# Optimization experiments

Hardware: AMD Instinct MI355X
Metric: run time of the kernel (lower is better)

## Reference

```python
import jax, jax.numpy as jnp
import numpy as np

B, T, S = 4, 1024, 1024
E, H, D, M = 768, 12, 64, 3072
SCALE = 1.0 / (D ** 0.5)
EPS = 1e-5


def setup_inputs() -> dict:
    key = jax.random.key(0)
    ks = jax.random.split(key, 20)
    s = 0.02

    def n(k, shp):
        return jax.random.normal(k, shp, jnp.float32) * s

    return {
        "target": jax.random.normal(ks[0], (B, T, E), jnp.float32),
        "memory": jax.random.normal(ks[1], (B, S, E), jnp.float32),
        # self-attention: per-head Q/K/V projections stacked over heads [H,E,D]
        "sa_wq": n(ks[2], (H, E, D)), "sa_bq": jnp.zeros((H, D), jnp.float32),
        "sa_wk": n(ks[3], (H, E, D)), "sa_bk": jnp.zeros((H, D), jnp.float32),
        "sa_wv": n(ks[4], (H, E, D)), "sa_bv": jnp.zeros((H, D), jnp.float32),
        "sa_wo": n(ks[5], (H * D, E)), "sa_bo": jnp.zeros((E,), jnp.float32),
        # cross-attention
        "ca_wq": n(ks[6], (H, E, D)), "ca_bq": jnp.zeros((H, D), jnp.float32),
        "ca_wk": n(ks[7], (H, E, D)), "ca_bk": jnp.zeros((H, D), jnp.float32),
        "ca_wv": n(ks[8], (H, E, D)), "ca_bv": jnp.zeros((H, D), jnp.float32),
        "ca_wo": n(ks[9], (H * D, E)), "ca_bo": jnp.zeros((E,), jnp.float32),
        # layernorms
        "ln1_g": jnp.ones((E,), jnp.float32), "ln1_b": jnp.zeros((E,), jnp.float32),
        "ln2_g": jnp.ones((E,), jnp.float32), "ln2_b": jnp.zeros((E,), jnp.float32),
        "ln3_g": jnp.ones((E,), jnp.float32), "ln3_b": jnp.zeros((E,), jnp.float32),
        # FFN
        "ffn_w1": n(ks[10], (E, M)), "ffn_b1": jnp.zeros((M,), jnp.float32),
        "ffn_w2": n(ks[11], (M, E)), "ffn_b2": jnp.zeros((E,), jnp.float32),
    }


def layernorm(x, g, b):
    mu = jnp.mean(x, axis=-1, keepdims=True)
    var = jnp.mean(jnp.square(x - mu), axis=-1, keepdims=True)
    return (x - mu) * jax.lax.rsqrt(var + EPS) * g + b


def mha(q_in, k_in, v_in, wq, bq, wk, bk, wv, bv, wo, bo, mask=None):
    # batched equivalent of the per-head looped projections
    Q = jnp.einsum('bse,hed->bhsd', q_in, wq) + bq[None, :, None, :]
    K = jnp.einsum('bte,hed->bhtd', k_in, wk) + bk[None, :, None, :]
    V = jnp.einsum('bte,hed->bhtd', v_in, wv) + bv[None, :, None, :]
    scores = jnp.einsum('bhsd,bhtd->bhst', Q, K) * SCALE
    if mask is not None:
        scores = jnp.where(mask, scores, -jnp.inf)
    w = jax.nn.softmax(scores, axis=-1)
    o = jnp.einsum('bhst,bhtd->bhsd', w, V)  # [B,H,Sq,D]
    o = o.transpose(0, 2, 1, 3).reshape(q_in.shape[0], q_in.shape[1], H * D)
    return o @ wo + bo


def reference(target, memory,
              sa_wq, sa_bq, sa_wk, sa_bk, sa_wv, sa_bv, sa_wo, sa_bo,
              ca_wq, ca_bq, ca_wk, ca_bk, ca_wv, ca_bv, ca_wo, ca_bo,
              ln1_g, ln1_b, ln2_g, ln2_b, ln3_g, ln3_b,
              ffn_w1, ffn_b1, ffn_w2, ffn_b2):
    Tq = target.shape[1]
    causal = jnp.tril(jnp.ones((Tq, Tq), bool))  # [T,T], broadcasts over B,H
    # pre-norm self-attention + residual
    x = layernorm(target, ln1_g, ln1_b)
    x = mha(x, x, x, sa_wq, sa_bq, sa_wk, sa_bk, sa_wv, sa_bv, sa_wo, sa_bo, causal) + target
    # pre-norm cross-attention + residual
    res = x
    y = layernorm(x, ln2_g, ln2_b)
    x = mha(y, memory, memory, ca_wq, ca_bq, ca_wk, ca_bk, ca_wv, ca_bv, ca_wo, ca_bo) + res
    # pre-norm FFN (Linear -> GELU -> Linear) + residual
    res = x
    y = layernorm(x, ln3_g, ln3_b)
    x = jax.nn.gelu(y @ ffn_w1 + ffn_b1) @ ffn_w2 + ffn_b2 + res
    return x
```

## Files before the change

kernel.cpp:

```cpp
#include <hip/hip_runtime.h>
#include <hip/hip_bf16.h>
#include <stdint.h>

#define BB 4
#define TT 1024
#define SS 1024
#define EE 768
#define HH 12
#define DDIM 64
#define MM 3072
#define NROWS 4096
#define ATT_SCALE 0.125f

typedef unsigned short u16;
using short8 = __attribute__((ext_vector_type(8))) short;
using f32x4  = __attribute__((ext_vector_type(4))) float;

__device__ inline f32x4 mfma16(short8 a, short8 b, f32x4 c) {
  return __builtin_amdgcn_mfma_f32_16x16x32_bf16(a, b, c, 0, 0, 0);
}

__device__ inline float b2f(u16 u) {
  union { uint32_t i; float f; } z; z.i = ((uint32_t)u) << 16; return z.f;
}
__device__ inline u16 f2b(float f) {
  __hip_bfloat16 h = __float2bfloat16(f);
  return *reinterpret_cast<u16*>(&h);
}
__device__ inline float loadf(const float* p) { return *p; }
__device__ inline float loadf(const u16* p) { return b2f(*p); }

__device__ inline float gelu_f(float x) {
  const float k0 = 0.7978845608028654f;
  const float k1 = 0.044715f;
  float t = tanhf(k0 * (x + k1 * x * x * x));
  return 0.5f * x * (1.0f + t);
}

__device__ inline void gload16(const u16* g, u16* l) {
  __builtin_amdgcn_global_load_lds(
      (const __attribute__((address_space(1))) unsigned int*)g,
      (__attribute__((address_space(3))) unsigned int*)l, 16, 0, 0);
}

__global__ __launch_bounds__(256) void prep_k(
    const float* __restrict__ target, const float* __restrict__ ln1_g,
    const float* __restrict__ ln1_b, u16* __restrict__ lnb,
    const float* __restrict__ mem, u16* __restrict__ memB,
    const float* __restrict__ bq3, const float* __restrict__ bk3,
    const float* __restrict__ bv3, float* __restrict__ d3,
    const float* __restrict__ bk2, const float* __restrict__ bv2,
    float* __restrict__ d2,
    const float* __restrict__ sa_wq, const float* __restrict__ sa_wk,
    const float* __restrict__ sa_wv, u16* __restrict__ wqkvT_sa,
    const float* __restrict__ ca_wq, const float* __restrict__ ca_wk,
    const float* __restrict__ ca_wv, u16* __restrict__ wqkvT_ca,
    const float* __restrict__ sa_wo, const float* __restrict__ ca_wo,
    u16* __restrict__ woT,
    const float* __restrict__ ffn_w1, u16* __restrict__ w1T,
    const float* __restrict__ ffn_w2, u16* __restrict__ w2T) {
  __shared__ u16 tile[32][34];
  __shared__ float red[8];
  const int blk = blockIdx.x, t = threadIdx.x;
  if (blk < 4096) {
    const float* xr = target + (size_t)blk * EE;
    float v0 = xr[t], v1 = xr[t + 256], v2 = xr[t + 512];
    float s = v0 + v1 + v2;
#pragma unroll
    for (int m = 32; m >= 1; m >>= 1) s += __shfl_xor(s, m);
    int wv = t >> 6, ln = t & 63;
    if (ln == 0) red[wv] = s;
    __syncthreads();
    float mean = (red[0] + red[1] + red[2] + red[3]) * (1.0f / EE);
    float e0 = v0 - mean, e1 = v1 - mean, e2 = v2 - mean;
    float s2 = e0 * e0 + e1 * e1 + e2 * e2;
#pragma unroll
    for (int m = 32; m >= 1; m >>= 1) s2 += __shfl_xor(s2, m);
    if (ln == 0) red[4 + wv] = s2;
    __syncthreads();
    float var = (red[4] + red[5] + red[6] + red[7]) * (1.0f / EE);
    float rstd = rsqrtf(var + 1e-5f);
    u16* yr = lnb + (size_t)blk * EE;
    yr[t]       = f2b(e0 * rstd * ln1_g[t]       + ln1_b[t]);
    yr[t + 256] = f2b(e1 * rstd * ln1_g[t + 256] + ln1_b[t + 256]);
    yr[t + 512] = f2b(e2 * rstd * ln1_g[t + 512] + ln1_b[t + 512]);
  } else if (blk < 7168) {
    int i = ((blk - 4096) * 256 + t) * 4;
    float4 f = *(const float4*)(mem + i);
    u16 o[4] = {f2b(f.x), f2b(f.y), f2b(f.z), f2b(f.w)};
    *(uint64_t*)(memB + i) = *(const uint64_t*)o;
  } else if (blk < 7177) {
    int i = (blk - 7168) * 256 + t;
    if (i < 768) d3[i] = bq3[i];
    else if (i < 1536) d3[i] = bk3[i - 768];
    else d3[i] = bv3[i - 1536];
  } else if (blk < 7183) {
    int i = (blk - 7177) * 256 + t;
    if (i < 768) d2[i] = bk2[i];
    else d2[i] = bv2[i - 768];
  } else {
    const float* ip; u16* op; int R, C, bx, by;
    int r = blk - 7183;
    if (r < 1728) {
      int u = r / 48, rr = r % 48; bx = rr & 1; by = rr >> 1;
      const float* s = (u < 12) ? sa_wq : (u < 24) ? sa_wk : sa_wv;
      ip = s + (size_t)(u % 12) * EE * DDIM;
      op = wqkvT_sa + (size_t)u * EE * DDIM;
      R = EE; C = DDIM;
    } else if (r < 3456) {
      r -= 1728;
      int u = r / 48, rr = r % 48; bx = rr & 1; by = rr >> 1;
      const float* s = (u < 12) ? ca_wq : (u < 24) ? ca_wk : ca_wv;
      ip = s + (size_t)(u % 12) * EE * DDIM;
      op = wqkvT_ca + (size_t)u * EE * DDIM;
      R = EE; C = DDIM;
    } else if (r < 4608) {
      r -= 3456;
      int u = r / 576, rr = r % 576; bx = rr % 24; by = rr / 24;
      ip = (u == 0) ? sa_wo : ca_wo;
      op = woT + (size_t)u * EE * EE;
      R = EE; C = EE;
    } else if (r < 6912) {
      r -= 4608; bx = r % 96; by = r / 96;
      ip = ffn_w1; op = w1T; R = EE; C = MM;
    } else {
      r -= 6912; bx = r % 24; by = r / 24;
      ip = ffn_w2; op = w2T; R = MM; C = EE;
    }
    int r0 = by * 32, c0 = bx * 32;
    int tx = t & 31, ty = t >> 5;
#pragma unroll
    for (int j = 0; j < 32; j += 8)
      tile[ty + j][tx] = f2b(ip[(size_t)(r0 + ty + j) * C + (c0 + tx)]);
    __syncthreads();
#pragma unroll
    for (int j = 0; j < 32; j += 8)
      op[(size_t)(c0 + ty + j) * R + (r0 + tx)] = tile[tx][ty + j];
  }
}

template <typename T>
__global__ __launch_bounds__(256) void layernorm_k(const T* __restrict__ x,
    const float* __restrict__ g, const float* __restrict__ b,
    u16* __restrict__ y) {
  int row = blockIdx.x, t = threadIdx.x;
  const T* xr = x + (size_t)row * EE;
  float v0 = loadf(xr + t), v1 = loadf(xr + t + 256), v2 = loadf(xr + t + 512);
  float s = v0 + v1 + v2;
#pragma unroll
  for (int m = 32; m >= 1; m >>= 1) s += __shfl_xor(s, m);
  __shared__ float red[8];
  int wv = t >> 6, ln = t & 63;
  if (ln == 0) red[wv] = s;
  __syncthreads();
  float mean = (red[0] + red[1] + red[2] + red[3]) * (1.0f / EE);
  float d0 = v0 - mean, d1 = v1 - mean, d2 = v2 - mean;
  float s2 = d0 * d0 + d1 * d1 + d2 * d2;
#pragma unroll
  for (int m = 32; m >= 1; m >>= 1) s2 += __shfl_xor(s2, m);
  if (ln == 0) red[4 + wv] = s2;
  __syncthreads();
  float var = (red[4] + red[5] + red[6] + red[7]) * (1.0f / EE);
  float rstd = rsqrtf(var + 1e-5f);
  u16* yr = y + (size_t)row * EE;
  yr[t]       = f2b(d0 * rstd * g[t]       + b[t]);
  yr[t + 256] = f2b(d1 * rstd * g[t + 256] + b[t + 256]);
  yr[t + 512] = f2b(d2 * rstd * g[t + 512] + b[t + 512]);
}

template <int RESMODE, bool GELU, bool XCDSWZ, typename OutT>
__global__ __launch_bounds__(256) void gemm128_k(
    const u16* __restrict__ A, const u16* __restrict__ Bt,
    const float* __restrict__ bias, const void* __restrict__ res,
    OutT* __restrict__ C, int M, int N, int K) {
  __shared__ u16 As[2][128 * 32];
  __shared__ u16 Bs[2][128 * 32];
  int bx = blockIdx.x, by = blockIdx.y;
  if (XCDSWZ) {
    const int nbx = N >> 7;
    int id = bx + nbx * by;
    int per = (nbx * (M >> 7)) >> 3;
    int sid = (id & 7) * per + (id >> 3);
    bx = sid % nbx; by = sid / nbx;
  }
  const int bm = by * 128, bn = bx * 128;
  const int t = threadIdx.x;
  const int wave = t >> 6, lane = t & 63;
  const int wr = wave >> 1, wc = wave & 1;
  const int g = lane >> 4, li = lane & 15;
  f32x4 acc[4][4] = {};
  const size_t rowskip = (size_t)64 * K;
  const int scol = (((t & 3) ^ ((t >> 3) & 3)) * 8);
  const u16* Ag = A + (size_t)(bm + (t >> 2)) * K + scol;
  const u16* Bg = Bt + (size_t)(bn + (t >> 2)) * K + scol;

  gload16(Ag, &As[0][t * 8]);
  gload16(Ag + rowskip, &As[0][2048 + t * 8]);
  gload16(Bg, &Bs[0][t * 8]);
  gload16(Bg + rowskip, &Bs[0][2048 + t * 8]);
  __syncthreads();

  const int nsteps = K >> 5;
  for (int s = 0; s < nsteps; s++) {
    const int cur = s & 1;
    if (s + 1 < nsteps) {
      const int k0 = (s + 1) << 5;
      gload16(Ag + k0, &As[cur ^ 1][t * 8]);
      gload16(Ag + rowskip + k0, &As[cur ^ 1][2048 + t * 8]);
      gload16(Bg + k0, &Bs[cur ^ 1][t * 8]);
      gload16(Bg + rowskip + k0, &Bs[cur ^ 1][2048 + t * 8]);
    }
    short8 af[4], bf[4];
#pragma unroll
    for (int i = 0; i < 4; i++) {
      const int ar = wr * 64 + i * 16 + li;
      af[i] = *(const short8*)(&As[cur][ar * 32 + ((g ^ ((ar >> 1) & 3)) * 8)]);
      const int br = wc * 64 + i * 16 + li;
      bf[i] = *(const short8*)(&Bs[cur][br * 32 + ((g ^ ((br >> 1) & 3)) * 8)]);
    }
#pragma unroll
    for (int mi = 0; mi < 4; mi++)
#pragma unroll
      for (int nj = 0; nj < 4; nj++)
        acc[mi][nj] = mfma16(af[mi], bf[nj], acc[mi][nj]);
    __syncthreads();
  }

#pragma unroll
  for (int mi = 0; mi < 4; mi++)
#pragma unroll
    for (int nj = 0; nj < 4; nj++) {
      int n = bn + wc * 64 + nj * 16 + li;
      float bv = bias[n];
#pragma unroll
      for (int i = 0; i < 4; i++) {
        int m = bm + wr * 64 + mi * 16 + g * 4 + i;
        float val = acc[mi][nj][i] + bv;
        if (GELU) val = gelu_f(val);
        if (RESMODE == 1) val += ((const float*)res)[(size_t)m * N + n];
        else if (RESMODE == 2) val += b2f(((const u16*)res)[(size_t)m * N + n]);
        if constexpr (sizeof(OutT) == 2) C[(size_t)m * N + n] = f2b(val);
        else                             C[(size_t)m * N + n] = val;
      }
    }
}

__global__ __launch_bounds__(256) void gemm128_dual_k(
    const u16* __restrict__ A0, const u16* __restrict__ B0,
    const float* __restrict__ bias0, u16* __restrict__ C0, int N0, int nbx0,
    const u16* __restrict__ A1, const u16* __restrict__ B1,
    const float* __restrict__ bias1, u16* __restrict__ C1, int N1,
    u16* __restrict__ vtsa, u16* __restrict__ vtca,
    int M, int K) {
  __shared__ u16 As[2][128 * 32];
  __shared__ u16 Bs[2][128 * 32];
  const int id = blockIdx.x + 30 * blockIdx.y;
  const int sid = (id & 7) * 120 + (id >> 3);
  const int x = sid % 30, y = sid / 30;
  const bool p1 = (x >= nbx0);
  const u16* A = p1 ? A1 : A0;
  const u16* Bt = p1 ? B1 : B0;
  const float* bias = p1 ? bias1 : bias0;
  u16* C = p1 ? C1 : C0;
  const int N = p1 ? N1 : N0;
  const int bn = (p1 ? x - nbx0 : x) * 128;
  const int bm = y * 128;
  const int t = threadIdx.x;
  const int wave = t >> 6, lane = t & 63;
  const int wr = wave >> 1, wc = wave & 1;
  const int g = lane >> 4, li = lane & 15;
  f32x4 acc[4][4] = {};
  const size_t rowskip = (size_t)64 * K;
  const int scol = (((t & 3) ^ ((t >> 3) & 3)) * 8);
  const u16* Ag = A + (size_t)(bm + (t >> 2)) * K + scol;
  const u16* Bg = Bt + (size_t)(bn + (t >> 2)) * K + scol;

  gload16(Ag, &As[0][t * 8]);
  gload16(Ag + rowskip, &As[0][2048 + t * 8]);
  gload16(Bg, &Bs[0][t * 8]);
  gload16(Bg + rowskip, &Bs[0][2048 + t * 8]);
  __syncthreads();

  const int nsteps = K >> 5;
  for (int s = 0; s < nsteps; s++) {
    const int cur = s & 1;
    if (s + 1 < nsteps) {
      const int k0 = (s + 1) << 5;
      gload16(Ag + k0, &As[cur ^ 1][t * 8]);
      gload16(Ag + rowskip + k0, &As[cur ^ 1][2048 + t * 8]);
      gload16(Bg + k0, &Bs[cur ^ 1][t * 8]);
      gload16(Bg + rowskip + k0, &Bs[cur ^ 1][2048 + t * 8]);
    }
    short8 af[4], bf[4];
#pragma unroll
    for (int i = 0; i < 4; i++) {
      const int ar = wr * 64 + i * 16 + li;
      af[i] = *(const short8*)(&As[cur][ar * 32 + ((g ^ ((ar >> 1) & 3)) * 8)]);
      const int br = wc * 64 + i * 16 + li;
      bf[i] = *(const short8*)(&Bs[cur][br * 32 + ((g ^ ((br >> 1) & 3)) * 8)]);
    }
#pragma unroll
    for (int mi = 0; mi < 4; mi++)
#pragma unroll
      for (int nj = 0; nj < 4; nj++)
        acc[mi][nj] = mfma16(af[mi], bf[nj], acc[mi][nj]);
    __syncthreads();
  }

  const int vbase = p1 ? 768 : 1536;
  u16* vtX = p1 ? vtca : vtsa;
  const bool isVblk = (bn >= vbase);

#pragma unroll
  for (int mi = 0; mi < 4; mi++)
#pragma unroll
    for (int nj = 0; nj < 4; nj++) {
      int n = bn + wc * 64 + nj * 16 + li;
      float bv = bias[n];
      u16 vv[4];
#pragma unroll
      for (int i = 0; i < 4; i++) {
        int m = bm + wr * 64 + mi * 16 + g * 4 + i;
        u16 o = f2b(acc[mi][nj][i] + bv);
        C[(size_t)m * N + n] = o;
        vv[i] = o;
      }
      if (isVblk) {
        int hd = n - vbase;
        int m0 = bm + wr * 64 + mi * 16 + g * 4;
        int bb = m0 >> 10, t0 = m0 & 1023;
        *(uint64_t*)(&vtX[((size_t)(bb * HH + (hd >> 6)) << 16) +
                          ((size_t)(hd & 63) << 10) + t0]) = *(const uint64_t*)vv;
      }
    }
}

template <int RESMODE, bool GELU, bool XCDSWZ, typename OutT>
__global__ __launch_bounds__(256) void gemm64_k(
    const u16* __restrict__ A, const u16* __restrict__ Bt,
    const float* __restrict__ bias, const void* __restrict__ res,
    OutT* __restrict__ C, int M, int N, int K) {
  __shared__ u16 As[2][64 * 64];
  __shared__ u16 Bs[2][64 * 64];
  int bx = blockIdx.x, by = blockIdx.y;
  if (XCDSWZ) {
    const int nbx = N >> 6;
    int id = bx + nbx * by;
    int per = (nbx * (M >> 6)) >> 3;
    int sid = (id & 7) * per + (id >> 3);
    bx = sid % nbx; by = sid / nbx;
  }
  const int bm = by * 64, bn = bx * 64;
  const int t = threadIdx.x;
  const int wave = t >> 6, lane = t & 63;
  const int wr = wave >> 1, wc = wave & 1;
  const int g = lane >> 4, li = lane & 15;
  f32x4 acc[2][2] = {};
  const int srow = t >> 3;
  const int scolz = ((t & 7) * 8) ^ ((srow & 7) << 3);
  const size_t skip32 = (size_t)32 * K;
  const u16* Ag = A + (size_t)(bm + srow) * K + scolz;
  const u16* Bg = Bt + (size_t)(bn + srow) * K + scolz;

  gload16(Ag, &As[0][t * 8]);
  gload16(Ag + skip32, &As[0][2048 + t * 8]);
  gload16(Bg, &Bs[0][t * 8]);
  gload16(Bg + skip32, &Bs[0][2048 + t * 8]);
  __syncthreads();

  const int nsteps = K >> 6;
  for (int s = 0; s < nsteps; s++) {
    const int cur = s & 1;
    if (s + 1 < nsteps) {
      const int k0 = (s + 1) << 6;
      gload16(Ag + k0, &As[cur ^ 1][t * 8]);
      gload16(Ag + skip32 + k0, &As[cur ^ 1][2048 + t * 8]);
      gload16(Bg + k0, &Bs[cur ^ 1][t * 8]);
      gload16(Bg + skip32 + k0, &Bs[cur ^ 1][2048 + t * 8]);
    }
    short8 af[2][2], bf[2][2];
#pragma unroll
    for (int mt = 0; mt < 2; mt++)
#pragma unroll
      for (int kk = 0; kk < 2; kk++) {
        int ar = wr * 32 + mt * 16 + li;
        af[mt][kk] = *(const short8*)(&As[cur][ar * 64 + ((kk * 32 + g * 8) ^ ((ar & 7) << 3))]);
        int br = wc * 32 + mt * 16 + li;
        bf[mt][kk] = *(const short8*)(&Bs[cur][br * 64 + ((kk * 32 + g * 8) ^ ((br & 7) << 3))]);
      }
#pragma unroll
    for (int mt = 0; mt < 2; mt++)
#pragma unroll
      for (int nt = 0; nt < 2; nt++)
#pragma unroll
        for (int kk = 0; kk < 2; kk++)
          acc[mt][nt] = mfma16(af[mt][kk], bf[nt][kk], acc[mt][nt]);
    __syncthreads();
  }

#pragma unroll
  for (int mt = 0; mt < 2; mt++)
#pragma unroll
    for (int nt = 0; nt < 2; nt++) {
      int n = bn + wc * 32 + nt * 16 + li;
      float bv = bias[n];
#pragma unroll
      for (int i = 0; i < 4; i++) {
        int m = bm + wr * 32 + mt * 16 + g * 4 + i;
        float val = acc[mt][nt][i] + bv;
        if (GELU) val = gelu_f(val);
        if (RESMODE == 1) val += ((const float*)res)[(size_t)m * N + n];
        else if (RESMODE == 2) val += b2f(((const u16*)res)[(size_t)m * N + n]);
        if constexpr (sizeof(OutT) == 2) C[(size_t)m * N + n] = f2b(val);
        else                             C[(size_t)m * N + n] = val;
      }
    }
}

template <bool CAUSAL>
__global__ __launch_bounds__(256) void attn4_k(
    const u16* __restrict__ Q, const u16* __restrict__ K,
    const u16* __restrict__ VT, u16* __restrict__ O,
    int ldq, int ldk) {
  int b, h, q0;
  if (CAUSAL) {
    int id = blockIdx.x;
    int cu = id & 255, slot = id >> 8;
    int q, hb;
    if (cu < 96) {
      int p = cu & 1, r = cu >> 1;
      q = (slot == 0 ? 0 : slot == 1 ? 6 : 14) + p;
      hb = r;
    } else if (cu < 192) {
      int c2 = cu - 96; int p = c2 & 1, r = c2 >> 1;
      q = (slot == 0 ? 2 : slot == 1 ? 8 : 12) + p;
      hb = r;
    } else if (cu < 224) {
      int c2 = cu - 192;
      int p = c2 & 1, r = c2 >> 1;
      if (slot == 0)      { q = 10;    hb = c2; }
      else if (slot == 1) { q = 11;    hb = c2; }
      else                { q = 4 + p; hb = r; }
    } else {
      int c2 = cu - 224;
      int p = c2 & 1, r = c2 >> 1;
      if (slot == 0)      { q = 4;      hb = 16 + c2; }
      else if (slot == 1) { q = 5;      hb = 16 + c2; }
      else                { q = 10 + p; hb = 32 + r; }
    }
    h = hb % HH; b = hb / HH; q0 = q * 64;
  } else {
    b = blockIdx.z; h = blockIdx.y; q0 = blockIdx.x * 64;
  }
  int tid = threadIdx.x, wave = tid >> 6, lane = tid & 63;
  int g = lane >> 4, li = lane & 15;
  const u16* Qb = Q + (size_t)b * TT * ldq + h * DDIM;
  const u16* Kb = K + (size_t)b * SS * ldk + h * DDIM;
  const u16* Vb = VT + (size_t)(b * HH + h) * DDIM * SS;
  u16* Ob = O + (size_t)b * TT * EE + h * DDIM;

  __shared__ u16 Ks[128 * 64];
  __shared__ u16 Vs[64 * 128];
  __shared__ u16 Ps[4][16][132];

  int qrow = q0 + wave * 16 + li;
  short8 qf0 = *(const short8*)(Qb + (size_t)qrow * ldq + g * 8);
  short8 qf1 = *(const short8*)(Qb + (size_t)qrow * ldq + 32 + g * 8);

  f32x4 accO[4] = {};
  float lrow[4] = {0.f, 0.f, 0.f, 0.f};

  const int krow = tid >> 3;
  const int vrow = tid >> 4;
  const int qmax = q0 + wave * 16 + 15;

  int kvEnd = CAUSAL ? (((q0 + 64 + 127) >> 7) << 7) : SS;
  for (int kv0 = 0; kv0 < kvEnd; kv0 += 128) {
#pragma unroll
    for (int j = 0; j < 4; j++) {
      int kr = j * 32 + krow;
      int kc = ((tid & 7) * 8) ^ ((kr & 7) << 3);
      gload16(Kb + (size_t)(kv0 + kr) * ldk + kc, &Ks[j * 2048 + tid * 8]);
    }
#pragma unroll
    for (int j = 0; j < 4; j++) {
      int vr = j * 16 + vrow;
      int vc = ((tid & 15) * 8) ^ ((vr & 15) << 3);
      gload16(Vb + (size_t)vr * SS + kv0 + vc, &Vs[j * 2048 + tid * 8]);
    }
    __syncthreads();

    if (!CAUSAL || kv0 <= qmax) {
      const bool needMask = CAUSAL && (kv0 + 127 > qmax);
      f32x4 s[8];
#pragma unroll
      for (int kt = 0; kt < 8; kt++) {
        int kr = kt * 16 + li;
        int sw = (kr & 7) << 3;
        short8 kf0 = *(const short8*)(&Ks[kr * 64 + ((g * 8) ^ sw)]);
        short8 kf1 = *(const short8*)(&Ks[kr * 64 + ((g * 8 + 32) ^ sw)]);
        f32x4 z = {};
        z = mfma16(qf0, kf0, z);
        z = mfma16(qf1, kf1, z);
        s[kt] = z;
      }

      float rsum[4] = {0.f, 0.f, 0.f, 0.f};
#pragma unroll
      for (int kt = 0; kt < 8; kt++)
#pragma unroll
        for (int i = 0; i < 4; i++) {
          float sv = s[kt][i] * ATT_SCALE;
          if (needMask) {
            int qi = q0 + wave * 16 + g * 4 + i;
            int ti = kv0 + kt * 16 + li;
            if (ti > qi) sv = -1e30f;
          }
          float p = __expf(sv);
          s[kt][i] = p;
          rsum[i] += p;
        }
#pragma unroll
      for (int msk = 1; msk < 16; msk <<= 1)
#pragma unroll
        for (int i = 0; i < 4; i++) rsum[i] += __shfl_xor(rsum[i], msk);
#pragma unroll
      for (int i = 0; i < 4; i++) lrow[i] += rsum[i];

#pragma unroll
      for (int kt = 0; kt < 8; kt++)
#pragma unroll
        for (int i = 0; i < 4; i++)
          Ps[wave][g * 4 + i][kt * 16 + li] = f2b(s[kt][i]);

#pragma unroll
      for (int tc = 0; tc < 4; tc++) {
        short8 pf = *(const short8*)(&Ps[wave][li][tc * 32 + g * 8]);
#pragma unroll
        for (int dt = 0; dt < 4; dt++) {
          int vr = dt * 16 + li;
          short8 vf = *(const short8*)(&Vs[vr * 128 + ((tc * 32 + g * 8) ^ ((vr & 15) << 3))]);
          accO[dt] = mfma16(pf, vf, accO[dt]);
        }
      }
    }
    __syncthreads();
  }

#pragma unroll
  for (int i = 0; i < 4; i++) {
    float inv = 1.0f / lrow[i];
    int q = q0 + wave * 16 + g * 4 + i;
#pragma unroll
    for (int dt = 0; dt < 4; dt++)
      Ob[(size_t)q * EE + dt * 16 + li] = f2b(accO[dt][i] * inv);
  }
}

static inline void* wsoff(void* ws, size_t& off, size_t bytes) {
  void* p = (char*)ws + off;
  off += (bytes + 255) & ~(size_t)255;
  return p;
}

extern "C" void kernel_launch(void* const* d_in, const int* in_sizes, int n_in,
                              void* d_out, int out_size, void* d_ws, size_t ws_size,
                              hipStream_t stream) {
  const float* target = (const float*)d_in[0];
  const float* memory = (const float*)d_in[1];
  const float* sa_wq = (const float*)d_in[2];  const float* sa_bq = (const float*)d_in[3];
  const float* sa_wk = (const float*)d_in[4];  const float* sa_bk = (const float*)d_in[5];
  const float* sa_wv = (const float*)d_in[6];  const float* sa_bv = (const float*)d_in[7];
  const float* sa_wo = (const float*)d_in[8];  const float* sa_bo = (const float*)d_in[9];
  const float* ca_wq = (const float*)d_in[10]; const float* ca_bq = (const float*)d_in[11];
  const float* ca_wk = (const float*)d_in[12]; const float* ca_bk = (const float*)d_in[13];
  const float* ca_wv = (const float*)d_in[14]; const float* ca_bv = (const float*)d_in[15];
  const float* ca_wo = (const float*)d_in[16]; const float* ca_bo = (const float*)d_in[17];
  const float* ln1_g = (const float*)d_in[18]; const float* ln1_b = (const float*)d_in[19];
  const float* ln2_g = (const float*)d_in[20]; const float* ln2_b = (const float*)d_in[21];
  const float* ln3_g = (const float*)d_in[22]; const float* ln3_b = (const float*)d_in[23];
  const float* ffn_w1 = (const float*)d_in[24]; const float* ffn_b1 = (const float*)d_in[25];
  const float* ffn_w2 = (const float*)d_in[26]; const float* ffn_b2 = (const float*)d_in[27];

  size_t off = 0;
  const size_t WB = (size_t)EE * EE * 2;
  u16* wqkvT_sa = (u16*)wsoff(d_ws, off, 3 * WB);
  u16* wqT_ca   = (u16*)wsoff(d_ws, off, WB);
  u16* wkvT_ca  = (u16*)wsoff(d_ws, off, 2 * WB);
  u16* woT_sa   = (u16*)wsoff(d_ws, off, WB);
  u16* woT_ca   = (u16*)wsoff(d_ws, off, WB);
  u16* w1T      = (u16*)wsoff(d_ws, off, (size_t)EE * MM * 2);
  u16* w2T      = (u16*)wsoff(d_ws, off, (size_t)EE * MM * 2);
  float* bsa_qkv = (float*)wsoff(d_ws, off, 2304 * 4);
  float* bca_kv  = (float*)wsoff(d_ws, off, 1536 * 4);
  const size_t AB = (size_t)NROWS * EE * 2;
  u16* mx2   = (u16*)wsoff(d_ws, off, AB);
  u16* lnb   = (u16*)wsoff(d_ws, off, AB);
  u16* S2    = (u16*)wsoff(d_ws, off, 3 * AB);
  u16* S3    = (u16*)wsoff(d_ws, off, AB);
  u16* x1    = (u16*)wsoff(d_ws, off, AB);
  u16* vtsa  = (u16*)wsoff(d_ws, off, AB);
  u16* vtca  = (u16*)wsoff(d_ws, off, AB);
  u16* kvca  = (u16*)wsoff(d_ws, off, 2 * AB);
  u16* qkv_sa = S2;
  u16* qb_ca  = S2;
  u16* attn_out = S3;
  u16* f1     = S2;
  u16* memB   = mx2;
  u16* x2     = mx2;

  prep_k<<<16399, 256, 0, stream>>>(
      target, ln1_g, ln1_b, lnb,
      memory, memB,
      sa_bq, sa_bk, sa_bv, bsa_qkv, ca_bk, ca_bv, bca_kv,
      sa_wq, sa_wk, sa_wv, wqkvT_sa,
      ca_wq, ca_wk, ca_wv, wqT_ca,
      sa_wo, ca_wo, woT_sa,
      ffn_w1, w1T, ffn_w2, w2T);

  gemm128_dual_k<<<dim3(30, 32), 256, 0, stream>>>(
      lnb, wqkvT_sa, bsa_qkv, qkv_sa, 3 * EE, 18,
      memB, wkvT_ca, bca_kv, kvca, 2 * EE,
      vtsa, vtca, NROWS, EE);

  attn4_k<true><<<dim3(768, 1, 1), 256, 0, stream>>>(
      qkv_sa, qkv_sa + EE, vtsa, attn_out, 3 * EE, 3 * EE);
  gemm64_k<1, false, true, u16><<<dim3(12, 64), 256, 0, stream>>>(
      attn_out, woT_sa, sa_bo, target, x1, NROWS, EE, EE);

  layernorm_k<u16><<<NROWS, 256, 0, stream>>>(x1, ln2_g, ln2_b, lnb);
  gemm64_k<0, false, true, u16><<<dim3(12, 64), 256, 0, stream>>>(
      lnb, wqT_ca, ca_bq, nullptr, qb_ca, NROWS, EE, EE);
  attn4_k<false><<<dim3(16, 12, 4), 256, 0, stream>>>(
      qb_ca, kvca, vtca, attn_out, EE, 2 * EE);
  gemm64_k<2, false, true, u16><<<dim3(12, 64), 256, 0, stream>>>(
      attn_out, woT_ca, ca_bo, x1, x2, NROWS, EE, EE);

  layernorm_k<u16><<<NROWS, 256, 0, stream>>>(x2, ln3_g, ln3_b, lnb);
  gemm128_k<0, true, true, u16><<<dim3(24, 32), 256, 0, stream>>>(
      lnb, w1T, ffn_b1, nullptr, f1, NROWS, MM, EE);
  gemm64_k<2, false, true, float><<<dim3(12, 64), 256, 0, stream>>>(
      f1, w2T, ffn_b2, x2, (float*)d_out, NROWS, EE, MM);
}
```

Measured before the change: 235.2 us.

## Stage V-transpose writes through LDS, swizzle attention blocks across XCDs, use exp2

```diff
diff --git a/kernel.cpp b/kernel.cpp
--- a/kernel.cpp
+++ b/kernel.cpp
@@ -10,7 +10,7 @@
 #define DDIM 64
 #define MM 3072
 #define NROWS 4096
-#define ATT_SCALE 0.125f
+#define SCALE2 0.18033688011112042f
 
 typedef unsigned short u16;
 using short8 = __attribute__((ext_vector_type(8))) short;
@@ -307,32 +307,51 @@
     __syncthreads();
   }
 
-  const int vbase = p1 ? 768 : 1536;
-  u16* vtX = p1 ? vtca : vtsa;
-  const bool isVblk = (bn >= vbase);
-
 #pragma unroll
   for (int mi = 0; mi < 4; mi++)
 #pragma unroll
     for (int nj = 0; nj < 4; nj++) {
       int n = bn + wc * 64 + nj * 16 + li;
       float bv = bias[n];
-      u16 vv[4];
 #pragma unroll
       for (int i = 0; i < 4; i++) {
         int m = bm + wr * 64 + mi * 16 + g * 4 + i;
-        u16 o = f2b(acc[mi][nj][i] + bv);
-        C[(size_t)m * N + n] = o;
-        vv[i] = o;
+        C[(size_t)m * N + n] = f2b(acc[mi][nj][i] + bv);
       }
-      if (isVblk) {
-        int hd = n - vbase;
-        int m0 = bm + wr * 64 + mi * 16 + g * 4;
-        int bb = m0 >> 10, t0 = m0 & 1023;
-        *(uint64_t*)(&vtX[((size_t)(bb * HH + (hd >> 6)) << 16) +
-                          ((size_t)(hd & 63) << 10) + t0]) = *(const uint64_t*)vv;
+    }
+
+  const int vbase = p1 ? 768 : 1536;
+  if (bn >= vbase) {
+    u16* vtX = p1 ? vtca : vtsa;
+    u16* tl = &As[0][0];
+    const int bb = bm >> 10;
+    const int t0b = bm & 1023;
+#pragma unroll
+    for (int nj = 0; nj < 4; nj++) {
+      __syncthreads();
+      {
+        int n = bn + wc * 64 + nj * 16 + li;
+        float bv = bias[n];
+#pragma unroll
+        for (int mi = 0; mi < 4; mi++)
+#pragma unroll
+          for (int i = 0; i < 4; i++) {
+            int ml = wr * 64 + mi * 16 + g * 4 + i;
+            tl[(wc * 16 + li) * 132 + ml] = f2b(acc[mi][nj][i] + bv);
+          }
       }
-    }
+      __syncthreads();
+      int lr = t >> 3, m0 = (t & 7) * 16;
+      int n = bn + (lr >> 4) * 64 + nj * 16 + (lr & 15);
+      int hd = n - vbase;
+      uint4 v0 = *(uint4*)&tl[lr * 132 + m0];
+      uint4 v1 = *(uint4*)&tl[lr * 132 + m0 + 8];
+      u16* dst = vtX + (((size_t)(bb * HH + (hd >> 6))) << 16) +
+                 ((size_t)(hd & 63) << 10) + t0b + m0;
+      *(uint4*)dst = v0;
+      *(uint4*)(dst + 8) = v1;
+    }
+  }
 }
 
 template <int RESMODE, bool GELU, bool XCDSWZ, typename OutT>
@@ -450,7 +469,11 @@
     }
     h = hb % HH; b = hb / HH; q0 = q * 64;
   } else {
-    b = blockIdx.z; h = blockIdx.y; q0 = blockIdx.x * 64;
+    int id = blockIdx.x + 16 * (blockIdx.y + HH * (int)blockIdx.z);
+    int sid = (id & 7) * 96 + (id >> 3);
+    q0 = (sid & 15) * 64;
+    int yz = sid >> 4;
+    h = yz % HH; b = yz / HH;
   }
   int tid = threadIdx.x, wave = tid >> 6, lane = tid & 63;
   int g = lane >> 4, li = lane & 15;
@@ -510,13 +533,13 @@
       for (int kt = 0; kt < 8; kt++)
 #pragma unroll
         for (int i = 0; i < 4; i++) {
-          float sv = s[kt][i] * ATT_SCALE;
+          float sv = s[kt][i] * SCALE2;
           if (needMask) {
             int qi = q0 + wave * 16 + g * 4 + i;
             int ti = kv0 + kt * 16 + li;
             if (ti > qi) sv = -1e30f;
           }
-          float p = __expf(sv);
+          float p = exp2f(sv);
           s[kt][i] = p;
           rsum[i] += p;
         }
```

Measured after the change: 231.7 us. About the same (-1.5%).
